# Performance work log

Measured on AMD Instinct MI355X. Metric: run time of the kernel, lower is better.

## Reference

```python
import jax, jax.numpy as jnp
import numpy as np

N_NODES = 100000
N_EDGES = 600000
EMB = 128
L = 5
NUM_ATOM = 119
NUM_CHIR = 3
NUM_BTYPE = 5
NUM_BDIR = 3
BN_EPS = 1e-5


def setup_inputs() -> dict:
    key = jax.random.key(0)
    ks = jax.random.split(key, 16)
    inp = {}
    inp['x'] = jax.random.randint(ks[0], (N_NODES, 2), 0, NUM_ATOM, dtype=jnp.int64 if jax.config.jax_enable_x64 else jnp.int32)
    inp['edge_index'] = jax.random.randint(ks[1], (2, N_EDGES), 0, N_NODES)
    inp['edge_attr'] = jax.random.randint(ks[2], (N_EDGES, 2), 0, NUM_BDIR)
    s = 0.05
    inp['x_emb1'] = jax.random.normal(ks[3], (NUM_ATOM, EMB), jnp.float32) * s
    inp['x_emb2'] = jax.random.normal(ks[4], (NUM_CHIR, EMB), jnp.float32) * s
    inp['edge_emb1'] = jax.random.normal(ks[5], (L, NUM_BTYPE, EMB), jnp.float32) * s
    inp['edge_emb2'] = jax.random.normal(ks[6], (L, NUM_BDIR, EMB), jnp.float32) * s
    inp['W1'] = jax.random.normal(ks[7], (L, EMB, 2 * EMB), jnp.float32) * (1.0 / np.sqrt(EMB))
    inp['b1'] = jnp.zeros((L, 2 * EMB), jnp.float32)
    inp['W2'] = jax.random.normal(ks[8], (L, 2 * EMB, EMB), jnp.float32) * (1.0 / np.sqrt(2 * EMB))
    inp['b2'] = jnp.zeros((L, EMB), jnp.float32)
    inp['eps'] = jnp.zeros((L,), jnp.float32)
    inp['gamma'] = jnp.ones((L, EMB), jnp.float32)
    inp['beta'] = jnp.zeros((L, EMB), jnp.float32)
    return inp


def reference(x, edge_index, edge_attr, x_emb1, x_emb2, edge_emb1, edge_emb2,
              W1, b1, W2, b2, eps, gamma, beta):
    N = x.shape[0]
    # node embedding: sum of two table lookups
    x0 = jnp.clip(x[:, 0], 0, x_emb1.shape[0] - 1)
    x1 = jnp.clip(x[:, 1], 0, x_emb2.shape[0] - 1)
    h = x_emb1[x0] + x_emb2[x1]  # [N, EMB]
    # add self loops (loop edge_attr = zeros -> bond type 0 / dir 0)
    loop = jnp.arange(N, dtype=edge_index.dtype)
    src = jnp.concatenate([edge_index[0], loop])  # [E+N]
    dst = jnp.concatenate([edge_index[1], loop])
    ea = jnp.concatenate([edge_attr, jnp.zeros((N, 2), dtype=edge_attr.dtype)], axis=0)
    e0 = jnp.clip(ea[:, 0], 0, edge_emb1.shape[1] - 1)
    e1 = jnp.clip(ea[:, 1], 0, edge_emb2.shape[1] - 1)
    n_layers = eps.shape[0]
    for i in range(n_layers):
        e = edge_emb1[i][e0] + edge_emb2[i][e1]              # [E+N, EMB]
        m = jax.nn.relu(h[src] + e)                           # gather + elementwise
        agg = jax.ops.segment_sum(m, dst, num_segments=N)     # scatter-add
        out = (1.0 + eps[i]) * h + agg
        # MLP: Linear -> ReLU -> Linear
        hmid = jax.nn.relu(out @ W1[i] + b1[i])
        h = hmid @ W2[i] + b2[i]
        # BatchNorm1d over nodes (batch statistics, biased variance)
        mean = jnp.mean(h, axis=0)
        var = jnp.mean((h - mean) ** 2, axis=0)
        h = (h - mean) * jax.lax.rsqrt(var + BN_EPS) * gamma[i] + beta[i]
        if i < n_layers - 1:
            h = jax.nn.relu(h)
    return h
```

## Files before the change

kernel.cpp:

```cpp
#include <hip/hip_runtime.h>

#define NN 100000
#define NPAD 100096
#define NE 600000
#define EMB 128

typedef unsigned short u16;
typedef unsigned int u32;
typedef unsigned long long u64;
typedef _Float16 half8 __attribute__((ext_vector_type(8)));
typedef float f32x4 __attribute__((ext_vector_type(4)));

__device__ __forceinline__ float4 ld4(const float* p) { return *(const float4*)p; }
__device__ __forceinline__ u32 packh2(float a, float b) {
  union { _Float16 h[2]; u32 d; } u;
  u.h[0] = (_Float16)a;
  u.h[1] = (_Float16)b;
  return u.d;
}

__global__ __launch_bounds__(256) void node_init_kernel(
    const int* __restrict__ x, const float* __restrict__ emb1,
    const float* __restrict__ emb2, _Float16* __restrict__ hb) {
  int tid = blockIdx.x * blockDim.x + threadIdx.x;
  int n = tid >> 4;
  if (n >= NN) return;
  int kc = tid & 15;
  int x0 = min(max(x[2 * n], 0), 118);
  int x1 = min(max(x[2 * n + 1], 0), 2);
  const float* p1 = emb1 + (size_t)x0 * EMB + kc * 8;
  const float* p2 = emb2 + (size_t)x1 * EMB + kc * 8;
  _Float16 o[8];
#pragma unroll
  for (int j = 0; j < 8; ++j) o[j] = (_Float16)(p1[j] + p2[j]);
  *(ulonglong2*)(hb + (size_t)n * EMB + kc * 8) = *(ulonglong2*)o;
}

__global__ __launch_bounds__(256) void hist_kernel(const int* __restrict__ ei,
                                                   int* __restrict__ deg) {
  int e = blockIdx.x * blockDim.x + threadIdx.x;
  if (e >= NE) return;
  atomicAdd(&deg[ei[NE + e]], 1);
}

__global__ __launch_bounds__(256) void scan1_kernel(const int* __restrict__ deg,
                                                    int* __restrict__ off,
                                                    int* __restrict__ bsum,
                                                    int* __restrict__ gbins) {
  __shared__ int s[256];
  __shared__ int l[33];
  int t = threadIdx.x;
  if (t < 33) l[t] = 0;
  int base = blockIdx.x * 1024 + t * 4;
  int v[4];
#pragma unroll
  for (int j = 0; j < 4; ++j) {
    int idx = base + j;
    v[j] = (idx < NN) ? deg[idx] : 0;
  }
  int tsum = v[0] + v[1] + v[2] + v[3];
  s[t] = tsum;
  __syncthreads();
  for (int d = 1; d < 256; d <<= 1) {
    int add = (t >= d) ? s[t - d] : 0;
    __syncthreads();
    s[t] += add;
    __syncthreads();
  }
  int run = s[t] - tsum;
#pragma unroll
  for (int j = 0; j < 4; ++j) {
    int idx = base + j;
    if (idx < NN) {
      off[idx] = run;
      atomicAdd(&l[32 - min(v[j], 32)], 1);
    }
    run += v[j];
  }
  if (t == 255) bsum[blockIdx.x] = s[255];
  __syncthreads();
  if (t < 33 && l[t]) atomicAdd(&gbins[t], l[t]);
}

__global__ void scan2_kernel(int* __restrict__ bsum, int* __restrict__ off, int nb,
                             int* __restrict__ gbins) {
  int t = threadIdx.x;
  if (t < 64) {
    int lane = t;
    int v0 = (lane < nb) ? bsum[lane] : 0;
    int v1 = (lane + 64 < nb) ? bsum[lane + 64] : 0;
    int s0 = v0, s1 = v1;
    for (int d = 1; d < 64; d <<= 1) {
      int t0 = __shfl_up(s0, d);
      int t1 = __shfl_up(s1, d);
      if (lane >= d) { s0 += t0; s1 += t1; }
    }
    int tot0 = __shfl(s0, 63);
    int tot1 = __shfl(s1, 63);
    if (lane < nb) bsum[lane] = s0 - v0;
    if (lane + 64 < nb) bsum[lane + 64] = tot0 + s1 - v1;
    if (lane == 0) off[NN] = tot0 + tot1;
  } else {
    int lane = t - 64;
    int v = (lane < 33) ? gbins[lane] : 0;
    int s = v;
    for (int d = 1; d < 64; d <<= 1) {
      int tt = __shfl_up(s, d);
      if (lane >= d) s += tt;
    }
    if (lane < 33) gbins[lane] = s - v;
  }
}

__global__ __launch_bounds__(256) void scan3_kernel(int* __restrict__ off,
                                                    const int* __restrict__ bsum,
                                                    const int* __restrict__ deg,
                                                    int* __restrict__ gbins,
                                                    int* __restrict__ perm) {
  __shared__ int lcnt[33], lbase[33];
  int t = threadIdx.x;
  if (t < 33) lcnt[t] = 0;
  __syncthreads();
  int idx = blockIdx.x * 256 + t;
  int b = 0, r = 0;
  if (idx < NN) {
    off[idx] += bsum[idx >> 10];
    b = 32 - min(deg[idx], 32);
    r = atomicAdd(&lcnt[b], 1);
  }
  __syncthreads();
  if (t < 33) lbase[t] = lcnt[t] ? atomicAdd(&gbins[t], lcnt[t]) : 0;
  __syncthreads();
  if (idx < NN) perm[lbase[b] + r] = idx;
}

__global__ __launch_bounds__(256) void scatter_kernel(
    const int* __restrict__ ei, const int* __restrict__ ea,
    const int* __restrict__ off, int* __restrict__ cnt, int* __restrict__ csr) {
  int e = blockIdx.x * blockDim.x + threadIdx.x;
  if (e >= NE) return;
  int d = ei[NE + e];
  int s = ei[e];
  int a0 = min(max(ea[2 * e], 0), 4);
  int a1 = min(max(ea[2 * e + 1], 0), 2);
  int code = a0 * 3 + a1;
  int r = atomicAdd(&cnt[d], 1);
  csr[off[d] + r] = s | (code << 20);
}

__global__ __launch_bounds__(256) void prep_kernel(
    const float* __restrict__ W1g, const float* __restrict__ W2g,
    const float* __restrict__ ee1, const float* __restrict__ ee2,
    _Float16* __restrict__ W1f, _Float16* __restrict__ W2f,
    _Float16* __restrict__ cbh) {
  int idx = blockIdx.x * blockDim.x + threadIdx.x;
  _Float16 o[8];
  if (idx < 20480) {
    int lane = idx & 63;
    int r = idx >> 6;
    int nt = r & 3, kt = (r >> 2) & 3, c = (r >> 4) & 3, l = r >> 6;
    int n = c * 64 + nt * 16 + (lane & 15);
    int kb = kt * 32 + (lane >> 4) * 8;
#pragma unroll
    for (int j = 0; j < 8; ++j) o[j] = (_Float16)W1g[((size_t)l * 128 + kb + j) * 256 + n];
    *(ulonglong2*)(W1f + (size_t)idx * 8) = *(ulonglong2*)o;
  } else if (idx < 40960) {
    int i2 = idx - 20480;
    int lane = i2 & 63;
    int r = i2 >> 6;
    int nt = r & 7, ktl = (r >> 3) & 1, c = (r >> 4) & 3, l = r >> 6;
    int n = nt * 16 + (lane & 15);
    int kb = c * 64 + ktl * 32 + (lane >> 4) * 8;
#pragma unroll
    for (int j = 0; j < 8; ++j) o[j] = (_Float16)W2g[((size_t)l * 256 + kb + j) * 128 + n];
    *(ulonglong2*)(W2f + (size_t)i2 * 8) = *(ulonglong2*)o;
  } else if (idx < 40960 + 9600) {
    int i3 = idx - 40960;
    int l = i3 / (15 * 128);
    int rem = i3 % (15 * 128);
    int code = rem / 128;
    int f = rem % 128;
    cbh[i3] = (_Float16)(ee1[(l * 5 + code / 3) * 128 + f] + ee2[(l * 3 + code % 3) * 128 + f]);
  }
}

template <bool NORM>
__global__ __launch_bounds__(256, 4) void fused_kernel(
    const _Float16* __restrict__ hsrc, const float* __restrict__ slots_prev,
    const float* __restrict__ gamma, const float* __restrict__ beta,
    const int* __restrict__ off, const int* __restrict__ csr,
    const _Float16* __restrict__ cbh, const float* __restrict__ epsp,
    const int* __restrict__ perm,
    const _Float16* __restrict__ W1f, const _Float16* __restrict__ W2f,
    const float* __restrict__ b1g, const float* __restrict__ b2g,
    _Float16* __restrict__ hout, float* __restrict__ slots_out) {
  __shared__ __align__(16) _Float16 Ws[16 * 64 * 8];
  __shared__ float s_sc[128], s_sh[128];

  const int t = threadIdx.x;
  const int w = t >> 6;
  const int lane = t & 63;
  const int q = lane >> 4, l15 = lane & 15;
  const int gw = blockIdx.x * 4 + w;
  const int n0 = gw * 16;
  float* sums = slots_out + (size_t)(gw & 31) * 256;

  if (NORM) {
    if (t < 128) {
      float s = 0.f, s2 = 0.f;
#pragma unroll 8
      for (int k = 0; k < 32; ++k) {
        s += slots_prev[k * 256 + t];
        s2 += slots_prev[k * 256 + 128 + t];
      }
      float mean = s * (1.0f / NN);
      float var = s2 * (1.0f / NN) - mean * mean;
      float sc = gamma[t] * rsqrtf(var + 1e-5f);
      s_sc[t] = sc;
      s_sh[t] = beta[t] - mean * sc;
    }
    __syncthreads();
  }

  {
    const int sub = q;
    const int kc = l15;
    float scv[8], shv[8];
    if (NORM) {
#pragma unroll
      for (int j = 0; j < 8; ++j) {
        scv[j] = s_sc[kc * 8 + j];
        shv[j] = s_sh[kc * 8 + j];
      }
    }
    const float eps1 = 1.0f + *epsp;
    half8 c0 = *(const half8*)(cbh + kc * 8);
    for (int p = 0; p < 4; ++p) {
      int g = n0 + p * 4 + sub;
      float av[8] = {0.f, 0.f, 0.f, 0.f, 0.f, 0.f, 0.f, 0.f};
      if (g < NN) {
        int node = perm[g];
        ulonglong2 hraw = *(const ulonglong2*)(hsrc + (size_t)node * EMB + kc * 8);
        _Float16* hr = (_Float16*)&hraw;
#pragma unroll
        for (int j = 0; j < 8; ++j) {
          float hv = (float)hr[j];
          if (NORM) hv = fmaxf(hv * scv[j] + shv[j], 0.f);
          av[j] = eps1 * hv + fmaxf(hv + (float)c0[j], 0.f);
        }
        int s0 = off[node], s1 = off[node + 1];
        int e = s0;
        for (; e + 3 < s1; e += 4) {
          int p0 = csr[e], p1 = csr[e + 1], p2 = csr[e + 2], p3 = csr[e + 3];
          ulonglong2 r0 = *(const ulonglong2*)(hsrc + (size_t)(p0 & 0xFFFFF) * EMB + kc * 8);
          ulonglong2 r1 = *(const ulonglong2*)(hsrc + (size_t)(p1 & 0xFFFFF) * EMB + kc * 8);
          ulonglong2 r2 = *(const ulonglong2*)(hsrc + (size_t)(p2 & 0xFFFFF) * EMB + kc * 8);
          ulonglong2 r3 = *(const ulonglong2*)(hsrc + (size_t)(p3 & 0xFFFFF) * EMB + kc * 8);
          ulonglong2 rr[4] = {r0, r1, r2, r3};
          int pp[4] = {p0, p1, p2, p3};
#pragma unroll
          for (int u = 0; u < 4; ++u) {
            half8 cc = *(const half8*)(cbh + (size_t)(pp[u] >> 20) * EMB + kc * 8);
            _Float16* sp = (_Float16*)&rr[u];
#pragma unroll
            for (int j = 0; j < 8; ++j) {
              float v = (float)sp[j];
              if (NORM) v = fmaxf(v * scv[j] + shv[j], 0.f);
              av[j] += fmaxf(v + (float)cc[j], 0.f);
            }
          }
        }
        for (; e < s1; ++e) {
          int p0 = csr[e];
          ulonglong2 r0 = *(const ulonglong2*)(hsrc + (size_t)(p0 & 0xFFFFF) * EMB + kc * 8);
          half8 cc = *(const half8*)(cbh + (size_t)(p0 >> 20) * EMB + kc * 8);
          _Float16* sp = (_Float16*)&r0;
#pragma unroll
          for (int j = 0; j < 8; ++j) {
            float v = (float)sp[j];
            if (NORM) v = fmaxf(v * scv[j] + shv[j], 0.f);
            av[j] += fmaxf(v + (float)cc[j], 0.f);
          }
        }
      }
      _Float16 o[8];
#pragma unroll
      for (int j = 0; j < 8; ++j) o[j] = (_Float16)av[j];
      *(ulonglong2*)&Ws[w * 2048 + (p * 4 + sub) * 128 + kc * 8] = *(ulonglong2*)o;
    }
  }

  half8 nh[4];
#pragma unroll
  for (int kt = 0; kt < 4; ++kt)
    nh[kt] = *(const half8*)&Ws[w * 2048 + l15 * 128 + kt * 32 + q * 8];

  f32x4 oacc[8];
#pragma unroll
  for (int a = 0; a < 8; ++a) oacc[a] = (f32x4){0.f, 0.f, 0.f, 0.f};

  const int srcA = ((q & 1) * 2) * 16 + l15;
  const int srcB = srcA + 16;
  const bool sel = (q >> 1) != 0;

  for (int c = 0; c < 4; ++c) {
    __syncthreads();
    {
      const _Float16* gb = W1f + ((size_t)(c * 16 + w * 4) * 64 + lane) * 8;
#pragma unroll
      for (int j = 0; j < 4; ++j)
        *(ulonglong2*)&Ws[(w * 4 + j) * 512 + lane * 8] =
            *(const ulonglong2*)(gb + (size_t)j * 512);
    }
    __syncthreads();

    f32x4 hacc[4];
#pragma unroll
    for (int a = 0; a < 4; ++a) hacc[a] = (f32x4){0.f, 0.f, 0.f, 0.f};
#pragma unroll
    for (int kt = 0; kt < 4; ++kt) {
#pragma unroll
      for (int colt = 0; colt < 4; ++colt) {
        half8 wh = *(const half8*)&Ws[(kt * 4 + colt) * 512 + lane * 8];
        hacc[colt] = __builtin_amdgcn_mfma_f32_16x16x32_f16(wh, nh[kt], hacc[colt], 0, 0, 0);
      }
    }
    __syncthreads();

    {
      const _Float16* gb = W2f + ((size_t)(c * 16 + w * 4) * 64 + lane) * 8;
#pragma unroll
      for (int j = 0; j < 4; ++j)
        *(ulonglong2*)&Ws[(w * 4 + j) * 512 + lane * 8] =
            *(const ulonglong2*)(gb + (size_t)j * 512);
    }

    u32 P01[4], P23[4];
#pragma unroll
    for (int colt = 0; colt < 4; ++colt) {
      float4 b1v = ld4(b1g + c * 64 + colt * 16 + q * 4);
      float v0 = fmaxf(hacc[colt][0] + b1v.x, 0.f);
      float v1 = fmaxf(hacc[colt][1] + b1v.y, 0.f);
      float v2 = fmaxf(hacc[colt][2] + b1v.z, 0.f);
      float v3 = fmaxf(hacc[colt][3] + b1v.w, 0.f);
      P01[colt] = packh2(v0, v1);
      P23[colt] = packh2(v2, v3);
    }
    __syncthreads();

#pragma unroll
    for (int ktl = 0; ktl < 2; ++ktl) {
      half8 bh;
      {
        union { u32 d[4]; half8 s; } uh;
        int c0 = 2 * ktl, c1 = 2 * ktl + 1;
        u32 a0, a1;
        a0 = (u32)__shfl((int)P01[c0], srcA); a1 = (u32)__shfl((int)P01[c1], srcA);
        uh.d[0] = sel ? a1 : a0;
        a0 = (u32)__shfl((int)P23[c0], srcA); a1 = (u32)__shfl((int)P23[c1], srcA);
        uh.d[1] = sel ? a1 : a0;
        a0 = (u32)__shfl((int)P01[c0], srcB); a1 = (u32)__shfl((int)P01[c1], srcB);
        uh.d[2] = sel ? a1 : a0;
        a0 = (u32)__shfl((int)P23[c0], srcB); a1 = (u32)__shfl((int)P23[c1], srcB);
        uh.d[3] = sel ? a1 : a0;
        bh = uh.s;
      }
#pragma unroll
      for (int nt = 0; nt < 8; ++nt) {
        half8 wh = *(const half8*)&Ws[(ktl * 8 + nt) * 512 + lane * 8];
        oacc[nt] = __builtin_amdgcn_mfma_f32_16x16x32_f16(wh, bh, oacc[nt], 0, 0, 0);
      }
    }
  }

  const int gg = n0 + l15;
  const bool ok = gg < NN;
  const int node = ok ? perm[gg] : 0;
#pragma unroll
  for (int nt = 0; nt < 8; ++nt) {
    int ocb = nt * 16 + q * 4;
    float4 b2v = ld4(b2g + ocb);
    f32x4 s = (f32x4){0.f, 0.f, 0.f, 0.f};
    f32x4 s2 = (f32x4){0.f, 0.f, 0.f, 0.f};
    if (ok) {
      float v0 = oacc[nt][0] + b2v.x;
      float v1 = oacc[nt][1] + b2v.y;
      float v2 = oacc[nt][2] + b2v.z;
      float v3 = oacc[nt][3] + b2v.w;
      u64 pk = (u64)packh2(v0, v1) | ((u64)packh2(v2, v3) << 32);
      *(u64*)(hout + (size_t)node * EMB + ocb) = pk;
      s[0] = v0; s[1] = v1; s[2] = v2; s[3] = v3;
      s2[0] = v0 * v0; s2[1] = v1 * v1; s2[2] = v2 * v2; s2[3] = v3 * v3;
    }
#pragma unroll
    for (int d = 1; d < 16; d <<= 1) {
#pragma unroll
      for (int r = 0; r < 4; ++r) {
        s[r] += __shfl_xor(s[r], d);
        s2[r] += __shfl_xor(s2[r], d);
      }
    }
    if (l15 == 0) {
#pragma unroll
      for (int r = 0; r < 4; ++r) {
        atomicAdd(&sums[ocb + r], s[r]);
        atomicAdd(&sums[128 + ocb + r], s2[r]);
      }
    }
  }
}

__global__ __launch_bounds__(256) void out_kernel(
    const _Float16* __restrict__ hpre, const float* __restrict__ slots,
    const float* __restrict__ gamma, const float* __restrict__ beta,
    float* __restrict__ out) {
  __shared__ float s_sc[128], s_sh[128];
  int t = threadIdx.x;
  if (t < 128) {
    float s = 0.f, s2 = 0.f;
#pragma unroll 8
    for (int k = 0; k < 32; ++k) {
      s += slots[k * 256 + t];
      s2 += slots[k * 256 + 128 + t];
    }
    float mean = s * (1.0f / NN);
    float var = s2 * (1.0f / NN) - mean * mean;
    float sc = gamma[t] * rsqrtf(var + 1e-5f);
    s_sc[t] = sc;
    s_sh[t] = beta[t] - mean * sc;
  }
  __syncthreads();
  int tid = blockIdx.x * blockDim.x + t;
  int n = tid >> 4;
  if (n >= NN) return;
  int kc = tid & 15;
  ulonglong2 raw = *(const ulonglong2*)(hpre + (size_t)n * EMB + kc * 8);
  _Float16* hr = (_Float16*)&raw;
  float v[8];
#pragma unroll
  for (int j = 0; j < 8; ++j) v[j] = (float)hr[j] * s_sc[kc * 8 + j] + s_sh[kc * 8 + j];
  float* d = out + (size_t)n * EMB + kc * 8;
  *(float4*)d = make_float4(v[0], v[1], v[2], v[3]);
  *(float4*)(d + 4) = make_float4(v[4], v[5], v[6], v[7]);
}

extern "C" void kernel_launch(void* const* d_in, const int* in_sizes, int n_in,
                              void* d_out, int out_size, void* d_ws, size_t ws_size,
                              hipStream_t stream) {
  const int* x = (const int*)d_in[0];
  const int* ei = (const int*)d_in[1];
  const int* ea = (const int*)d_in[2];
  const float* x_emb1 = (const float*)d_in[3];
  const float* x_emb2 = (const float*)d_in[4];
  const float* ee1 = (const float*)d_in[5];
  const float* ee2 = (const float*)d_in[6];
  const float* W1 = (const float*)d_in[7];
  const float* b1 = (const float*)d_in[8];
  const float* W2 = (const float*)d_in[9];
  const float* b2 = (const float*)d_in[10];
  const float* eps = (const float*)d_in[11];
  const float* gamma = (const float*)d_in[12];
  const float* beta = (const float*)d_in[13];
  float* out = (float*)d_out;

  float* slots = (float*)d_ws;
  _Float16* hp0 = (_Float16*)(slots + 5 * 32 * 256);
  _Float16* hp1 = hp0 + (size_t)NN * EMB;
  _Float16* hb = hp1 + (size_t)NN * EMB;
  _Float16* W1f = hb + (size_t)NN * EMB;
  _Float16* W2f = W1f + 5 * 32768;
  _Float16* cbh = W2f + 5 * 32768;
  int* deg = (int*)(cbh + 5 * 15 * 128 + 64);
  int* off = deg + NN;
  int* csr = off + NN + 1;
  int* bsum = csr + NE;
  int* gbins = bsum + 128;
  int* perm = gbins + 64;

  const int NB_SCAN = (NN + 1023) / 1024;

  hipMemsetAsync(deg, 0, NN * sizeof(int), stream);
  hipMemsetAsync(gbins, 0, 64 * sizeof(int), stream);
  hipMemsetAsync(slots, 0, 5 * 32 * 256 * sizeof(float), stream);
  hist_kernel<<<(NE + 255) / 256, 256, 0, stream>>>(ei, deg);
  scan1_kernel<<<NB_SCAN, 256, 0, stream>>>(deg, off, bsum, gbins);
  scan2_kernel<<<1, 128, 0, stream>>>(bsum, off, NB_SCAN, gbins);
  scan3_kernel<<<(NN + 255) / 256, 256, 0, stream>>>(off, bsum, deg, gbins, perm);
  hipMemsetAsync(deg, 0, NN * sizeof(int), stream);
  scatter_kernel<<<(NE + 255) / 256, 256, 0, stream>>>(ei, ea, off, deg, csr);
  prep_kernel<<<(40960 + 9600 + 255) / 256, 256, 0, stream>>>(W1, W2, ee1, ee2, W1f,
                                                              W2f, cbh);
  node_init_kernel<<<NN * 16 / 256 + 1, 256, 0, stream>>>(x, x_emb1, x_emb2, hb);

  const int NBLK = NPAD / 64;
  for (int i = 0; i < 5; ++i) {
    const _Float16* hin = (i == 0) ? hb : ((i & 1) ? hp0 : hp1);
    _Float16* hout = (i & 1) ? hp1 : hp0;
    if (i == 0)
      fused_kernel<false><<<NBLK, 256, 0, stream>>>(
          hin, nullptr, nullptr, nullptr, off, csr, cbh, eps, perm,
          W1f, W2f, b1, b2, hout, slots);
    else
      fused_kernel<true><<<NBLK, 256, 0, stream>>>(
          hin, slots + (size_t)(i - 1) * 32 * 256, gamma + (size_t)(i - 1) * EMB,
          beta + (size_t)(i - 1) * EMB, off, csr, cbh + (size_t)i * 15 * EMB,
          eps + i, perm, W1f + (size_t)i * 32768, W2f + (size_t)i * 32768,
          b1 + (size_t)i * 256, b2 + (size_t)i * 128, hout,
          slots + (size_t)i * 32 * 256);
  }
  out_kernel<<<NN * 16 / 256 + 1, 256, 0, stream>>>(
      hp0, slots + 4 * 32 * 256, gamma + 4 * EMB, beta + 4 * EMB, out);
}
```

Measured before the change: 601.4 us.

## Pad CSR rows to multiples of 8 with dummy edges to drop remainder loop

Each node's CSR segment is rounded up to a multiple of 8 and filled with a dummy entry. The dummy points at a zeroed padding row of h and at a sentinel edge-code row of -60000, so its relu contribution is zero. The gather loop becomes a fully unrolled 8-wide loop with no remainder branch, which gives more memory-level parallelism per iteration. In exchange the CSR array grows, padded entries cost wasted gathers, and scan3 now launches over the whole CSR capacity to initialise it.

```diff
diff --git a/kernel.cpp b/kernel.cpp
--- a/kernel.cpp
+++ b/kernel.cpp
@@ -3,7 +3,9 @@
 #define NN 100000
 #define NPAD 100096
 #define NE 600000
+#define CSRCAP (NE + 7 * NN)
 #define EMB 128
+#define DUMMY (NN | (15 << 20))
 
 typedef unsigned short u16;
 typedef unsigned int u32;
@@ -52,13 +54,14 @@
   int t = threadIdx.x;
   if (t < 33) l[t] = 0;
   int base = blockIdx.x * 1024 + t * 4;
-  int v[4];
+  int v[4], p[4];
 #pragma unroll
   for (int j = 0; j < 4; ++j) {
     int idx = base + j;
     v[j] = (idx < NN) ? deg[idx] : 0;
-  }
-  int tsum = v[0] + v[1] + v[2] + v[3];
+    p[j] = (v[j] + 7) & ~7;
+  }
+  int tsum = p[0] + p[1] + p[2] + p[3];
   s[t] = tsum;
   __syncthreads();
   for (int d = 1; d < 256; d <<= 1) {
@@ -75,7 +78,7 @@
       off[idx] = run;
       atomicAdd(&l[32 - min(v[j], 32)], 1);
     }
-    run += v[j];
+    run += p[j];
   }
   if (t == 255) bsum[blockIdx.x] = s[255];
   __syncthreads();
@@ -116,12 +119,14 @@
                                                     const int* __restrict__ bsum,
                                                     const int* __restrict__ deg,
                                                     int* __restrict__ gbins,
-                                                    int* __restrict__ perm) {
+                                                    int* __restrict__ perm,
+                                                    int* __restrict__ csr) {
   __shared__ int lcnt[33], lbase[33];
   int t = threadIdx.x;
   if (t < 33) lcnt[t] = 0;
   __syncthreads();
   int idx = blockIdx.x * 256 + t;
+  if (idx < CSRCAP) csr[idx] = DUMMY;
   int b = 0, r = 0;
   if (idx < NN) {
     off[idx] += bsum[idx >> 10];
@@ -174,13 +179,16 @@
 #pragma unroll
     for (int j = 0; j < 8; ++j) o[j] = (_Float16)W2g[((size_t)l * 256 + kb + j) * 128 + n];
     *(ulonglong2*)(W2f + (size_t)i2 * 8) = *(ulonglong2*)o;
-  } else if (idx < 40960 + 9600) {
+  } else if (idx < 40960 + 5 * 16 * 128) {
     int i3 = idx - 40960;
-    int l = i3 / (15 * 128);
-    int rem = i3 % (15 * 128);
-    int code = rem / 128;
-    int f = rem % 128;
-    cbh[i3] = (_Float16)(ee1[(l * 5 + code / 3) * 128 + f] + ee2[(l * 3 + code % 3) * 128 + f]);
+    int l = i3 / (16 * 128);
+    int rem = i3 % (16 * 128);
+    int code = rem >> 7;
+    int f = rem & 127;
+    cbh[i3] = (code < 15)
+                  ? (_Float16)(ee1[(l * 5 + code / 3) * 128 + f] +
+                               ee2[(l * 3 + code % 3) * 128 + f])
+                  : (_Float16)(-60000.0f);
   }
 }
 
@@ -248,18 +256,17 @@
           if (NORM) hv = fmaxf(hv * scv[j] + shv[j], 0.f);
           av[j] = eps1 * hv + fmaxf(hv + (float)c0[j], 0.f);
         }
-        int s0 = off[node], s1 = off[node + 1];
-        int e = s0;
-        for (; e + 3 < s1; e += 4) {
-          int p0 = csr[e], p1 = csr[e + 1], p2 = csr[e + 2], p3 = csr[e + 3];
-          ulonglong2 r0 = *(const ulonglong2*)(hsrc + (size_t)(p0 & 0xFFFFF) * EMB + kc * 8);
-          ulonglong2 r1 = *(const ulonglong2*)(hsrc + (size_t)(p1 & 0xFFFFF) * EMB + kc * 8);
-          ulonglong2 r2 = *(const ulonglong2*)(hsrc + (size_t)(p2 & 0xFFFFF) * EMB + kc * 8);
-          ulonglong2 r3 = *(const ulonglong2*)(hsrc + (size_t)(p3 & 0xFFFFF) * EMB + kc * 8);
-          ulonglong2 rr[4] = {r0, r1, r2, r3};
-          int pp[4] = {p0, p1, p2, p3};
-#pragma unroll
-          for (int u = 0; u < 4; ++u) {
+        const int s1 = off[node + 1];
+        for (int e = off[node]; e < s1; e += 8) {
+          int pp[8];
+#pragma unroll
+          for (int u = 0; u < 8; ++u) pp[u] = csr[e + u];
+          ulonglong2 rr[8];
+#pragma unroll
+          for (int u = 0; u < 8; ++u)
+            rr[u] = *(const ulonglong2*)(hsrc + (size_t)(pp[u] & 0xFFFFF) * EMB + kc * 8);
+#pragma unroll
+          for (int u = 0; u < 8; ++u) {
             half8 cc = *(const half8*)(cbh + (size_t)(pp[u] >> 20) * EMB + kc * 8);
             _Float16* sp = (_Float16*)&rr[u];
 #pragma unroll
@@ -268,18 +275,6 @@
               if (NORM) v = fmaxf(v * scv[j] + shv[j], 0.f);
               av[j] += fmaxf(v + (float)cc[j], 0.f);
             }
-          }
-        }
-        for (; e < s1; ++e) {
-          int p0 = csr[e];
-          ulonglong2 r0 = *(const ulonglong2*)(hsrc + (size_t)(p0 & 0xFFFFF) * EMB + kc * 8);
-          half8 cc = *(const half8*)(cbh + (size_t)(p0 >> 20) * EMB + kc * 8);
-          _Float16* sp = (_Float16*)&r0;
-#pragma unroll
-          for (int j = 0; j < 8; ++j) {
-            float v = (float)sp[j];
-            if (NORM) v = fmaxf(v * scv[j] + shv[j], 0.f);
-            av[j] += fmaxf(v + (float)cc[j], 0.f);
           }
         }
       }
@@ -465,15 +460,15 @@
 
   float* slots = (float*)d_ws;
   _Float16* hp0 = (_Float16*)(slots + 5 * 32 * 256);
-  _Float16* hp1 = hp0 + (size_t)NN * EMB;
-  _Float16* hb = hp1 + (size_t)NN * EMB;
-  _Float16* W1f = hb + (size_t)NN * EMB;
+  _Float16* hp1 = hp0 + (size_t)(NN + 1) * EMB;
+  _Float16* hb = hp1 + (size_t)(NN + 1) * EMB;
+  _Float16* W1f = hb + (size_t)(NN + 1) * EMB;
   _Float16* W2f = W1f + 5 * 32768;
   _Float16* cbh = W2f + 5 * 32768;
-  int* deg = (int*)(cbh + 5 * 15 * 128 + 64);
+  int* deg = (int*)(cbh + 5 * 16 * 128);
   int* off = deg + NN;
   int* csr = off + NN + 1;
-  int* bsum = csr + NE;
+  int* bsum = csr + CSRCAP;
   int* gbins = bsum + 128;
   int* perm = gbins + 64;
 
@@ -482,14 +477,18 @@
   hipMemsetAsync(deg, 0, NN * sizeof(int), stream);
   hipMemsetAsync(gbins, 0, 64 * sizeof(int), stream);
   hipMemsetAsync(slots, 0, 5 * 32 * 256 * sizeof(float), stream);
+  hipMemsetAsync(hp0 + (size_t)NN * EMB, 0, EMB * sizeof(_Float16), stream);
+  hipMemsetAsync(hp1 + (size_t)NN * EMB, 0, EMB * sizeof(_Float16), stream);
+  hipMemsetAsync(hb + (size_t)NN * EMB, 0, EMB * sizeof(_Float16), stream);
   hist_kernel<<<(NE + 255) / 256, 256, 0, stream>>>(ei, deg);
   scan1_kernel<<<NB_SCAN, 256, 0, stream>>>(deg, off, bsum, gbins);
   scan2_kernel<<<1, 128, 0, stream>>>(bsum, off, NB_SCAN, gbins);
-  scan3_kernel<<<(NN + 255) / 256, 256, 0, stream>>>(off, bsum, deg, gbins, perm);
+  scan3_kernel<<<(CSRCAP + 255) / 256, 256, 0, stream>>>(off, bsum, deg, gbins, perm,
+                                                         csr);
   hipMemsetAsync(deg, 0, NN * sizeof(int), stream);
   scatter_kernel<<<(NE + 255) / 256, 256, 0, stream>>>(ei, ea, off, deg, csr);
-  prep_kernel<<<(40960 + 9600 + 255) / 256, 256, 0, stream>>>(W1, W2, ee1, ee2, W1f,
-                                                              W2f, cbh);
+  prep_kernel<<<(40960 + 5 * 16 * 128 + 255) / 256, 256, 0, stream>>>(
+      W1, W2, ee1, ee2, W1f, W2f, cbh);
   node_init_kernel<<<NN * 16 / 256 + 1, 256, 0, stream>>>(x, x_emb1, x_emb2, hb);
 
   const int NBLK = NPAD / 64;
@@ -503,7 +502,7 @@
     else
       fused_kernel<true><<<NBLK, 256, 0, stream>>>(
           hin, slots + (size_t)(i - 1) * 32 * 256, gamma + (size_t)(i - 1) * EMB,
-          beta + (size_t)(i - 1) * EMB, off, csr, cbh + (size_t)i * 15 * EMB,
+          beta + (size_t)(i - 1) * EMB, off, csr, cbh + (size_t)i * 16 * EMB,
           eps + i, perm, W1f + (size_t)i * 32768, W2f + (size_t)i * 32768,
           b1 + (size_t)i * 256, b2 + (size_t)i * 128, hout,
           slots + (size_t)i * 32 * 256);
```

Result: slower. 658.7 us (+9.5%).
